# Kernel optimization log

Measured on AMD Instinct MI355X. Metric: run time of the kernel, lower is better.

## Reference

```python
import jax, jax.numpy as jnp
import numpy as np
import math

TWO_PI = 2.0 * math.pi
NBINS = 36  # num_ang_bins


def circular_gauss_kernel(kernlen=32):
    half = kernlen / 2.0
    r2 = half * half
    sigma2 = 0.9 * r2
    ys, xs = np.mgrid[0:kernlen, 0:kernlen].astype(np.float64)
    disq = (ys - half) ** 2 + (xs - half) ** 2
    k = np.where(disq < r2, np.exp(-disq / sigma2), 0.0)
    return k.astype(np.float32)


def setup_inputs() -> dict:
    key = jax.random.key(0)
    B, PS = 65536, 32
    x = jax.random.normal(key, (B, 1, PS, PS), dtype=jnp.float32)
    gx_w = jnp.array([0.5, 0.0, -0.5], dtype=jnp.float32)   # 1x3 gradient kernel
    gy_w = jnp.array([0.5, 0.0, -0.5], dtype=jnp.float32)   # 3x1 gradient kernel
    smooth_w = jnp.array([0.33, 0.34, 0.33], dtype=jnp.float32)  # angular smoothing
    gk = 10.0 * jnp.asarray(circular_gauss_kernel(PS))      # [PS, PS]
    return {"x": x, "gx_w": gx_w, "gy_w": gy_w, "smooth_w": smooth_w, "gk": gk}


def reference(x, gx_w, gy_w, smooth_w, gk):
    B, _, H, W = x.shape
    # horizontal gradient: replicate-pad width, cross-correlate [0.5, 0, -0.5]
    xp = jnp.pad(x, ((0, 0), (0, 0), (0, 0), (1, 1)), mode='edge')
    gx = gx_w[0] * xp[:, :, :, :-2] + gx_w[1] * xp[:, :, :, 1:-1] + gx_w[2] * xp[:, :, :, 2:]
    # vertical gradient: replicate-pad height
    yp = jnp.pad(x, ((0, 0), (0, 0), (1, 1), (0, 0)), mode='edge')
    gy = gy_w[0] * yp[:, :, :-2, :] + gy_w[1] * yp[:, :, 1:-1, :] + gy_w[2] * yp[:, :, 2:, :]
    mag = jnp.sqrt(gx * gx + gy * gy + 1e-10) * gk[None, None]
    keep = (mag > 0.001).astype(x.dtype)
    gx = gx * keep
    gy = gy * keep
    mag = mag * keep
    ori = jnp.arctan2(gy, gx)
    # torch wraps o_big in torch.tensor(...) which detaches it -> stop_gradient
    o_big = jax.lax.stop_gradient(NBINS * jnp.mod(ori, TWO_PI) / TWO_PI)
    bo0f = jnp.floor(o_big)
    wo1 = o_big - bo0f
    bo0 = jnp.mod(bo0f, NBINS).astype(jnp.int32)  # bin index per pixel
    wo0 = (1.0 - wo1) * mag                       # weight (original uses only wo0 in histogram)
    # fused soft histogram: per-patch scatter-add over 36 bins, then mean over HW
    ids = (jnp.arange(B, dtype=jnp.int32)[:, None] * NBINS + bo0.reshape(B, -1)).reshape(-1)
    hist = jax.ops.segment_sum(wo0.reshape(-1), ids, num_segments=B * NBINS)
    hist = hist.reshape(B, NBINS) / (H * W)  # adaptive_avg_pool2d to (1,1)
    # conv1d kernel-3, zero padding=1 angular smoothing
    hp = jnp.pad(hist, ((0, 0), (1, 1)))
    sm = smooth_w[0] * hp[:, :-2] + smooth_w[1] * hp[:, 1:-1] + smooth_w[2] * hp[:, 2:]
    idx = jnp.argmax(sm, axis=1)
    angle = -(TWO_PI * idx.astype(x.dtype) / NBINS - math.pi)
    return angle
```

## Files before the change

### kernel.cpp

```cpp
#include <hip/hip_runtime.h>
#include <math.h>

#define NBINS 36
#define TWO_PI_F 6.28318530717958647692f
#define PI_F     3.14159265358979323846f

#pragma clang fp contract(off)

__device__ __forceinline__ float atan2f_cr(float fy, float fx) {
    const double gy = (double)fy, gx = (double)fx;
    const double ay = fabs(gy), ax = fabs(gx);
    const double mx = fmax(ax, ay), mn = fmin(ax, ay);
    const bool hi = mn > 0.41421356237309503 * mx;
    const double num = hi ? mn - mx : mn;
    const double den = hi ? mn + mx : mx;
    const double u = num / den;
    const double z = u * u;
    const double w = z * z;
    const double s1 = z * __builtin_fma(w, __builtin_fma(w, __builtin_fma(w,
        __builtin_fma(w, __builtin_fma(w, 1.62858201153657823623e-02,
                                          4.97687799461593236017e-02),
                                          6.66107313738753120669e-02),
                                          9.09088713343650656196e-02),
                                          1.42857142725034663711e-01),
                                          3.33333333333329318027e-01);
    const double s2 = w * __builtin_fma(w, __builtin_fma(w, __builtin_fma(w,
        __builtin_fma(w, -3.65315727442169155270e-02,
                         -5.83357013379057348645e-02),
                         -7.69187620504482999495e-02),
                         -1.11111104054623557880e-01),
                         -1.99999999998764832476e-01);
    double phi = u - u * (s1 + s2);
    if (hi) phi = 0.78539816339744830962 + phi;
    if (ay > ax) phi = 1.57079632679489661923 - phi;
    if (__float_as_uint(fx) & 0x80000000u)
        phi = 3.14159265358979323846 - phi;
    if (__float_as_uint(fy) & 0x80000000u)
        phi = -phi;
    const float c1 = (float)(phi * (1.0 - 7.5e-14));
    const float c2 = (float)(phi * (1.0 + 7.5e-14));
    if (__builtin_expect(c1 != c2, 0))
        return (float)atan2(gy, gx);
    return c1;
}

__global__ __launch_bounds__(256, 2) void orient_kernel(
    const float* __restrict__ x,
    const float* __restrict__ gxw_p,
    const float* __restrict__ gyw_p,
    const float* __restrict__ sww_p,
    const float* __restrict__ gk,
    float* __restrict__ out)
{
#pragma clang fp contract(off)
    __shared__ float          rowbuf[4][64][33];
    __shared__ float          w_rec[2][64][33];
    __shared__ unsigned char  bin_rec[2][64][33];
    __shared__ float          acc[64][37];
    __shared__ float          gk_s[1024];

    const int tid = threadIdx.x;
    const size_t patch0 = (size_t)blockIdx.x * 64;

    const float gw0 = gxw_p[0], gw1 = gxw_p[1], gw2 = gxw_p[2];
    const float vw0 = gyw_p[0], vw1 = gyw_p[1], vw2 = gyw_p[2];

    ((float4*)gk_s)[tid] = ((const float4*)gk)[tid];
    for (int i = tid; i < 64 * 37; i += 256) ((float*)acc)[i] = 0.0f;
    for (int k = tid; k < 1536; k += 256) {
        const int row = k >> 9;
        const int rem = k & 511;
        const int pp  = rem >> 3;
        const int c4  = rem & 7;
        const float4 v = *((const float4*)(x + (patch0 + pp) * 1024 + row * 32 + c4 * 4));
        float* dst = &rowbuf[row][pp][c4 * 4];
        dst[0] = v.x; dst[1] = v.y; dst[2] = v.z; dst[3] = v.w;
    }
    __syncthreads();

    const int p  = tid >> 2;
    const int q  = tid & 3;
    const int rr = q >> 1;
    const int c0 = (q & 1) << 4;

    for (int ch = 0; ch < 16; ++ch) {
        {
            const int r  = 2 * ch + rr;
            const int su = (r == 0) ? 0 : ((r - 1) & 3);
            const int sc = r & 3;
            const int sd = (r + 1) & 3;
            float ctr  = rowbuf[sc][p][c0];
            float left = (c0 == 0) ? ctr : rowbuf[sc][p][c0 - 1];
            for (int i = 0; i < 16; ++i) {
                const int c = c0 + i;
                const float up    = rowbuf[su][p][c];
                const float dn    = rowbuf[sd][p][c];
                const float right = (c == 31) ? ctr : rowbuf[sc][p][c + 1];
                float gx  = gw0 * left + gw1 * ctr + gw2 * right;
                float gy  = vw0 * up   + vw1 * ctr + vw2 * dn;
                float ss  = gx * gx + gy * gy + 1e-10f;
                float mag = sqrtf(ss) * gk_s[(r << 5) + c];
                float wgt = 0.0f;
                int   bin = 0;
                if (mag > 0.001f) {
                    float o = atan2f_cr(gy, gx);
                    if (o < 0.0f) o += TWO_PI_F;
                    float obig = (36.0f * o) / TWO_PI_F;
                    float bof  = floorf(obig);
                    float fr   = obig - bof;
                    bin = (int)bof;
                    if (bin >= NBINS) bin = 0;
                    wgt = (1.0f - fr) * mag;
                }
                w_rec[rr][p][c]   = wgt;
                bin_rec[rr][p][c] = (unsigned char)bin;
                left = ctr; ctr = right;
            }
        }
        __syncthreads();

        if (tid < 64) {
            for (int rm = 0; rm < 2; ++rm) {
                for (int c = 0; c < 32; ++c) {
                    const float wv = w_rec[rm][tid][c];
                    const int   bv = bin_rec[rm][tid][c];
                    atomicAdd(&acc[tid][bv], wv);
                }
            }
        } else if (ch < 15) {
            for (int k = tid - 64; k < 1024; k += 192) {
                const int rowi = 2 * ch + 3 + (k >> 9);
                const int srow = rowi > 31 ? 31 : rowi;
                const int slot = rowi & 3;
                const int rem  = k & 511;
                const int pp   = rem >> 3;
                const int c4   = rem & 7;
                const float4 v = *((const float4*)(x + (patch0 + pp) * 1024 + srow * 32 + c4 * 4));
                float* dst = &rowbuf[slot][pp][c4 * 4];
                dst[0] = v.x; dst[1] = v.y; dst[2] = v.z; dst[3] = v.w;
            }
        }
        __syncthreads();
    }

    if (tid < 64) {
        const float s0 = sww_p[0], s1 = sww_p[1], s2 = sww_p[2];
        float hprev = 0.0f;
        float hc    = acc[tid][0] * (1.0f / 1024.0f);
        float best  = -1e30f;
        int   bi    = 0;
        for (int i = 0; i < NBINS; ++i) {
            const float hn = (i < NBINS - 1) ? acc[tid][i + 1] * (1.0f / 1024.0f) : 0.0f;
            const float sm = s0 * hprev + s1 * hc + s2 * hn;
            if (sm > best) { best = sm; bi = i; }
            hprev = hc; hc = hn;
        }
        float t = TWO_PI_F * (float)bi;
        t = t / 36.0f;
        out[patch0 + tid] = -(t - PI_F);
    }
}

extern "C" void kernel_launch(void* const* d_in, const int* in_sizes, int n_in,
                              void* d_out, int out_size, void* d_ws, size_t ws_size,
                              hipStream_t stream) {
    const float* x   = (const float*)d_in[0];
    const float* gxw = (const float*)d_in[1];
    const float* gyw = (const float*)d_in[2];
    const float* sw  = (const float*)d_in[3];
    const float* gk  = (const float*)d_in[4];
    float* out = (float*)d_out;

    const int nblocks = out_size / 64;
    orient_kernel<<<nblocks, 256, 0, stream>>>(x, gxw, gyw, sw, gk, out);
}
```

Baseline: 759.7 us.

## Warp-specialize loader/histogram wave and double-buffer per-row records

Result: slower. 807.7 us (+6.3%).

```diff
diff --git a/kernel.cpp b/kernel.cpp
--- a/kernel.cpp
+++ b/kernel.cpp
@@ -44,7 +44,7 @@
     return c1;
 }
 
-__global__ __launch_bounds__(256, 2) void orient_kernel(
+__global__ __launch_bounds__(192, 4) void orient_kernel(
     const float* __restrict__ x,
     const float* __restrict__ gxw_p,
     const float* __restrict__ gyw_p,
@@ -53,23 +53,24 @@
     float* __restrict__ out)
 {
 #pragma clang fp contract(off)
-    __shared__ float          rowbuf[4][64][33];
-    __shared__ float          w_rec[2][64][33];
-    __shared__ unsigned char  bin_rec[2][64][33];
-    __shared__ float          acc[64][37];
+    __shared__ float          rowbuf[4][32][33];
+    __shared__ float          w_rec[2][2][32][33];
+    __shared__ unsigned char  bin_rec[2][2][32][33];
+    __shared__ float          acc[32][37];
     __shared__ float          gk_s[1024];
 
     const int tid = threadIdx.x;
-    const size_t patch0 = (size_t)blockIdx.x * 64;
+    const size_t patch0 = (size_t)blockIdx.x * 32;
 
     const float gw0 = gxw_p[0], gw1 = gxw_p[1], gw2 = gxw_p[2];
     const float vw0 = gyw_p[0], vw1 = gyw_p[1], vw2 = gyw_p[2];
 
-    ((float4*)gk_s)[tid] = ((const float4*)gk)[tid];
-    for (int i = tid; i < 64 * 37; i += 256) ((float*)acc)[i] = 0.0f;
-    for (int k = tid; k < 1536; k += 256) {
-        const int row = k >> 9;
-        const int rem = k & 511;
+    for (int i = tid; i < 256; i += 192)
+        ((float4*)gk_s)[i] = ((const float4*)gk)[i];
+    for (int i = tid; i < 32 * 37; i += 192) ((float*)acc)[i] = 0.0f;
+    for (int k = tid; k < 768; k += 192) {
+        const int row = k >> 8;
+        const int rem = k & 255;
         const int pp  = rem >> 3;
         const int c4  = rem & 7;
         const float4 v = *((const float4*)(x + (patch0 + pp) * 1024 + row * 32 + c4 * 4));
@@ -78,17 +79,43 @@
     }
     __syncthreads();
 
-    const int p  = tid >> 2;
-    const int q  = tid & 3;
+    const int pt = tid - 64;
+    const int p  = pt >> 2;
+    const int q  = pt & 3;
     const int rr = q >> 1;
     const int c0 = (q & 1) << 4;
 
     for (int ch = 0; ch < 16; ++ch) {
-        {
+        float4 pre[8];
+        if (tid < 64) {
+            if (ch < 15) {
+#pragma unroll
+                for (int j = 0; j < 8; ++j) {
+                    const int k    = tid + 64 * j;
+                    const int rowi = 2 * ch + 3 + (k >> 8);
+                    const int srow = rowi > 31 ? 31 : rowi;
+                    const int rem  = k & 255;
+                    const int pp   = rem >> 3;
+                    const int c4   = rem & 7;
+                    pre[j] = *((const float4*)(x + (patch0 + pp) * 1024 + srow * 32 + c4 * 4));
+                }
+            }
+            if (ch > 0 && tid < 32) {
+                const int b = (ch - 1) & 1;
+                for (int rm = 0; rm < 2; ++rm) {
+                    for (int c = 0; c < 32; ++c) {
+                        const float wv = w_rec[b][rm][tid][c];
+                        const int   bv = bin_rec[b][rm][tid][c];
+                        atomicAdd(&acc[tid][bv], wv);
+                    }
+                }
+            }
+        } else {
             const int r  = 2 * ch + rr;
             const int su = (r == 0) ? 0 : ((r - 1) & 3);
             const int sc = r & 3;
             const int sd = (r + 1) & 3;
+            const int bf = ch & 1;
             float ctr  = rowbuf[sc][p][c0];
             float left = (c0 == 0) ? ctr : rowbuf[sc][p][c0 - 1];
             for (int i = 0; i < 16; ++i) {
@@ -112,38 +139,41 @@
                     if (bin >= NBINS) bin = 0;
                     wgt = (1.0f - fr) * mag;
                 }
-                w_rec[rr][p][c]   = wgt;
-                bin_rec[rr][p][c] = (unsigned char)bin;
+                w_rec[bf][rr][p][c]   = wgt;
+                bin_rec[bf][rr][p][c] = (unsigned char)bin;
                 left = ctr; ctr = right;
             }
         }
         __syncthreads();
 
-        if (tid < 64) {
-            for (int rm = 0; rm < 2; ++rm) {
-                for (int c = 0; c < 32; ++c) {
-                    const float wv = w_rec[rm][tid][c];
-                    const int   bv = bin_rec[rm][tid][c];
-                    atomicAdd(&acc[tid][bv], wv);
-                }
-            }
-        } else if (ch < 15) {
-            for (int k = tid - 64; k < 1024; k += 192) {
-                const int rowi = 2 * ch + 3 + (k >> 9);
-                const int srow = rowi > 31 ? 31 : rowi;
+        if (tid < 64 && ch < 15) {
+#pragma unroll
+            for (int j = 0; j < 8; ++j) {
+                const int k    = tid + 64 * j;
+                const int rowi = 2 * ch + 3 + (k >> 8);
                 const int slot = rowi & 3;
-                const int rem  = k & 511;
+                const int rem  = k & 255;
                 const int pp   = rem >> 3;
                 const int c4   = rem & 7;
-                const float4 v = *((const float4*)(x + (patch0 + pp) * 1024 + srow * 32 + c4 * 4));
                 float* dst = &rowbuf[slot][pp][c4 * 4];
-                dst[0] = v.x; dst[1] = v.y; dst[2] = v.z; dst[3] = v.w;
+                dst[0] = pre[j].x; dst[1] = pre[j].y; dst[2] = pre[j].z; dst[3] = pre[j].w;
             }
         }
         __syncthreads();
     }
 
-    if (tid < 64) {
+    if (tid < 32) {
+        for (int rm = 0; rm < 2; ++rm) {
+            for (int c = 0; c < 32; ++c) {
+                const float wv = w_rec[1][rm][tid][c];
+                const int   bv = bin_rec[1][rm][tid][c];
+                atomicAdd(&acc[tid][bv], wv);
+            }
+        }
+    }
+    __syncthreads();
+
+    if (tid < 32) {
         const float s0 = sww_p[0], s1 = sww_p[1], s2 = sww_p[2];
         float hprev = 0.0f;
         float hc    = acc[tid][0] * (1.0f / 1024.0f);
@@ -171,6 +201,6 @@
     const float* gk  = (const float*)d_in[4];
     float* out = (float*)d_out;
 
-    const int nblocks = out_size / 64;
-    orient_kernel<<<nblocks, 256, 0, stream>>>(x, gxw, gyw, sw, gk, out);
+    const int nblocks = out_size / 32;
+    orient_kernel<<<nblocks, 192, 0, stream>>>(x, gxw, gyw, sw, gk, out);
 }
```
